# Performance work log

Measured on AMD Instinct MI355X. Metric: run time of the kernel, lower is better.

Reference implementation:

```python
import jax, jax.numpy as jnp
import numpy as np

NEG_SLOPE = 0.2


def _gat_layer(x, src, dst, n, W, a_src, a_dst, b, concat):
    """PyG-style GATConv (inference, self-loops already in src/dst).
    x: [N, Fin]; W: [Fin, H*C]; a_src/a_dst: [H, C]; b: [H*C] or [C]."""
    H, C = a_src.shape
    h = (x @ W).reshape(-1, H, C)                      # [N, H, C]
    al_s = jnp.einsum('nhc,hc->nh', h, a_src)          # [N, H]
    al_d = jnp.einsum('nhc,hc->nh', h, a_dst)          # [N, H]
    e = al_s[src] + al_d[dst]                          # [E, H]
    e = jnp.where(e >= 0, e, NEG_SLOPE * e)            # LeakyReLU(0.2)
    m = jax.ops.segment_max(e, dst, num_segments=n)    # [N, H] softmax over dst
    e = jnp.exp(e - m[dst])
    s = jax.ops.segment_sum(e, dst, num_segments=n)    # [N, H]
    alpha = e / (s[dst] + 1e-16)                       # [E, H]
    msg = h[src] * alpha[:, :, None]                   # [E, H, C]
    out = jax.ops.segment_sum(msg, dst, num_segments=n)  # [N, H, C]
    if concat:
        out = out.reshape(-1, H * C)
    else:
        out = out.mean(axis=1)
    return out + b


def _forward(x, edge_index, W1, as1, ad1, b1, W2, as2, ad2, b2, W3, as3, ad3, b3):
    n = x.shape[0]
    loops = jnp.arange(n, dtype=edge_index.dtype)
    src = jnp.concatenate([edge_index[0], loops])      # add self-loops (PyG default)
    dst = jnp.concatenate([edge_index[1], loops])
    x = _gat_layer(x, src, dst, n, W1, as1, ad1, b1, concat=True)
    x = jax.nn.elu(x)
    x = _gat_layer(x, src, dst, n, W2, as2, ad2, b2, concat=True)
    x = jax.nn.elu(x)
    x = _gat_layer(x, src, dst, n, W3, as3, ad3, b3, concat=False)
    return x


def setup_inputs() -> dict:
    key = jax.random.key(0)
    ks = jax.random.split(key, 16)
    N, E, FIN, HID, H, OUT = 50000, 320000, 256, 64, 4, 64
    sc = 0.1  # keep attention logits in a sane range
    return {
        'x': jax.random.normal(ks[0], (N, FIN), jnp.float32),
        'edge_index': jax.random.randint(ks[1], (2, E), 0, N, jnp.int32),
        'W1': jax.random.normal(ks[2], (FIN, H * HID), jnp.float32) * sc,
        'as1': jax.random.normal(ks[3], (H, HID), jnp.float32) * sc,
        'ad1': jax.random.normal(ks[4], (H, HID), jnp.float32) * sc,
        'b1': jax.random.normal(ks[5], (H * HID,), jnp.float32) * sc,
        'W2': jax.random.normal(ks[6], (H * HID, H * HID), jnp.float32) * sc,
        'as2': jax.random.normal(ks[7], (H, HID), jnp.float32) * sc,
        'ad2': jax.random.normal(ks[8], (H, HID), jnp.float32) * sc,
        'b2': jax.random.normal(ks[9], (H * HID,), jnp.float32) * sc,
        'W3': jax.random.normal(ks[10], (H * HID, OUT), jnp.float32) * sc,
        'as3': jax.random.normal(ks[11], (1, OUT), jnp.float32) * sc,
        'ad3': jax.random.normal(ks[12], (1, OUT), jnp.float32) * sc,
        'b3': jax.random.normal(ks[13], (OUT,), jnp.float32) * sc,
    }


def reference(x, edge_index, W1, as1, ad1, b1, W2, as2, ad2, b2, W3, as3, ad3, b3):
    return _forward(x, edge_index, W1, as1, ad1, b1, W2, as2, ad2, b2, W3, as3, ad3, b3)
```

## Files before the change

### kernel.cpp

```cpp
#include <hip/hip_runtime.h>


typedef __attribute__((ext_vector_type(8))) __bf16 bf16x8;
typedef __attribute__((ext_vector_type(4))) float f32x4;
typedef _Float16 f16x8 __attribute__((ext_vector_type(8)));
typedef _Float16 f16x4 __attribute__((ext_vector_type(4)));

#define NEG_SLOPE 0.2f
#define WELL 40

__device__ __forceinline__ unsigned short f2b_rne(float f) {
    unsigned int u = __float_as_uint(f);
    u += 0x7FFFu + ((u >> 16) & 1u);
    return (unsigned short)(u >> 16);
}
__device__ __forceinline__ unsigned short f2h(float f) {
    _Float16 h = (_Float16)f;
    unsigned short s;
    __builtin_memcpy(&s, &h, 2);
    return s;
}
__device__ __forceinline__ bf16x8 cvt8(const float* f) {
    unsigned short r[8];
#pragma unroll
    for (int j = 0; j < 8; j++) r[j] = f2b_rne(f[j]);
    bf16x8 v;
    __builtin_memcpy(&v, r, 16);
    return v;
}
__device__ __forceinline__ float lrelu(float e) {
    return e >= 0.f ? e : NEG_SLOPE * e;
}

__global__ __launch_bounds__(256) void k_init(const float* __restrict__ W1,
                                              const float* __restrict__ W2,
                                              const float* __restrict__ W3,
                                              unsigned short* __restrict__ W1t,
                                              unsigned short* __restrict__ W2t,
                                              unsigned short* __restrict__ W3t,
                                              int* __restrict__ cnt, int n) {
    int t = blockIdx.x * blockDim.x + threadIdx.x;
    if (t < n) cnt[t] = 0;
    const float* W;
    unsigned short* Wt;
    int Nout, idx = t;
    if (idx < 65536)        { W = W1; Wt = W1t; Nout = 256; }
    else if (idx < 131072)  { W = W2; Wt = W2t; Nout = 256; idx -= 65536; }
    else if (idx < 147456)  { W = W3; Wt = W3t; Nout = 64;  idx -= 131072; }
    else return;
    int k = idx / Nout;
    int c = idx - k * Nout;
    Wt[(size_t)c * 256 + k] = f2b_rne(W[idx]);
}

__global__ __launch_bounds__(256) void k_fillell(const int* __restrict__ src,
                                                 const int* __restrict__ dst,
                                                 int* __restrict__ cnt,
                                                 int* __restrict__ ell, int E) {
    int t = blockIdx.x * blockDim.x + threadIdx.x;
    if (t < E) {
        int d = dst[t];
        int pos = atomicAdd(&cnt[d], 1);
        if (pos < WELL) ell[(size_t)d * WELL + pos] = src[t];
    }
}

template <int NT, bool AF32>
__global__ __launch_bounds__(512) void k_gemm(const void* __restrict__ Av,
                                              const __bf16* __restrict__ Bt,
                                              unsigned short* __restrict__ h16,
                                              float* __restrict__ als,
                                              float* __restrict__ ald,
                                              const float* __restrict__ a_s,
                                              const float* __restrict__ a_d,
                                              int M, int H) {
    constexpr int NN = NT * 16;
    __shared__ __align__(16) __bf16 Bs[NN][256];

    const int tid = threadIdx.x;
    const int lane = tid & 63;
    const int w = tid >> 6;
    const int i = lane & 15;
    const int quad = lane >> 4;
    const int m0 = blockIdx.x * 256;

    {
        int nl = lane >> 5;
        int p = lane & 31;
#pragma unroll
        for (int t = 0; t < NN / 16; t++) {
            int n = t * 16 + w * 2 + nl;
            int g = p ^ (n & 7);
            const __bf16* gp = Bt + (size_t)n * 256 + g * 8;
            __builtin_amdgcn_global_load_lds(
                (const __attribute__((address_space(1))) void*)gp,
                (__attribute__((address_space(3))) void*)&Bs[t * 16 + w * 2][0],
                16, 0, 0);
        }
    }

    int ra = m0 + w * 32 + i;
    int rb = ra + 16;
    if (ra >= M) ra = M - 1;
    if (rb >= M) rb = M - 1;

    bf16x8 afrag[2][8];
    if (AF32) {
        const float* pa = (const float*)Av + (size_t)ra * 256;
        const float* pb = (const float*)Av + (size_t)rb * 256;
#pragma unroll
        for (int half = 0; half < 2; half++) {
            float tmp[2][4][8];
#pragma unroll
            for (int k4 = 0; k4 < 4; k4++) {
                int koff = (half * 4 + k4) * 32 + quad * 8;
                *(float4*)&tmp[0][k4][0] = *(const float4*)(pa + koff);
                *(float4*)&tmp[0][k4][4] = *(const float4*)(pa + koff + 4);
                *(float4*)&tmp[1][k4][0] = *(const float4*)(pb + koff);
                *(float4*)&tmp[1][k4][4] = *(const float4*)(pb + koff + 4);
            }
#pragma unroll
            for (int k4 = 0; k4 < 4; k4++) {
                afrag[0][half * 4 + k4] = cvt8(tmp[0][k4]);
                afrag[1][half * 4 + k4] = cvt8(tmp[1][k4]);
            }
        }
    } else {
        const __bf16* pa = (const __bf16*)Av + (size_t)ra * 256;
        const __bf16* pb = (const __bf16*)Av + (size_t)rb * 256;
#pragma unroll
        for (int kc = 0; kc < 8; kc++) {
            int koff = kc * 32 + quad * 8;
            afrag[0][kc] = *(const bf16x8*)(pa + koff);
            afrag[1][kc] = *(const bf16x8*)(pb + koff);
        }
    }

    f32x4 acc[2][NT] = {};

    __syncthreads();

#pragma unroll
    for (int kc = 0; kc < 8; kc++) {
        const int c = kc * 4 + quad;
#pragma unroll
        for (int nt = 0; nt < NT; nt++) {
            const int n = nt * 16 + i;
            const int p = c ^ (n & 7);
            bf16x8 bfv = *(const bf16x8*)&Bs[n][p * 8];
            acc[0][nt] = __builtin_amdgcn_mfma_f32_16x16x32_bf16(
                afrag[0][kc], bfv, acc[0][nt], 0, 0, 0);
            acc[1][nt] = __builtin_amdgcn_mfma_f32_16x16x32_bf16(
                afrag[1][kc], bfv, acc[1][nt], 0, 0, 0);
        }
    }

    float asv[NT], adv[NT];
#pragma unroll
    for (int nt = 0; nt < NT; nt++) {
        asv[nt] = a_s[(nt / 4) * 64 + (nt & 3) * 16 + i];
        adv[nt] = a_d[(nt / 4) * 64 + (nt & 3) * 16 + i];
    }

#pragma unroll
    for (int mt = 0; mt < 2; mt++) {
#pragma unroll
        for (int r = 0; r < 4; r++) {
            int row = m0 + w * 32 + mt * 16 + quad * 4 + r;
            bool ok = row < M;
#pragma unroll
            for (int nt = 0; nt < NT; nt++) {
                if (ok) h16[(size_t)row * NN + nt * 16 + i] = f2h(acc[mt][nt][r]);
            }
#pragma unroll
            for (int g = 0; g < (NT + 3) / 4; g++) {
                float ps = 0.f, pd = 0.f;
#pragma unroll
                for (int j = 0; j < 4 && g * 4 + j < NT; j++) {
                    float v = acc[mt][g * 4 + j][r];
                    ps += v * asv[g * 4 + j];
                    pd += v * adv[g * 4 + j];
                }
#pragma unroll
                for (int off = 1; off <= 8; off <<= 1) {
                    ps += __shfl_xor(ps, off, 64);
                    pd += __shfl_xor(pd, off, 64);
                }
                if (ok && i == 0) {
                    als[(size_t)row * H + g] = ps;
                    ald[(size_t)row * H + g] = pd;
                }
            }
        }
    }
}

__global__ __launch_bounds__(256) void k_agg4(const unsigned short* __restrict__ h16,
                                              const float* __restrict__ als,
                                              const float* __restrict__ ald,
                                              const int* __restrict__ cnt,
                                              const int* __restrict__ ell,
                                              const float* __restrict__ bias,
                                              unsigned short* __restrict__ xout,
                                              int n) {
    int gw = (blockIdx.x * blockDim.x + threadIdx.x) >> 6;
    int lane = threadIdx.x & 63;
    int wid = gw * 4 + (lane >> 4);
    if (wid >= n) return;
    int l = lane & 15;
    int head = l >> 2;
    int ch = l * 16;
    int base = lane & 48;

    int deg = min(cnt[wid], WELL);
    const int* row = ell + (size_t)wid * WELL;
    int myid = (l < deg) ? row[l] : 0;

    float aldv = ald[wid * 4 + head];
    float p = __expf(fminf(lrelu(als[wid * 4 + head] + aldv), 60.f));
    float ssum = p;
    float a[16];
    {
        f16x8 h0 = *(const f16x8*)&h16[(size_t)wid * 256 + ch];
        f16x8 h1 = *(const f16x8*)&h16[(size_t)wid * 256 + ch + 8];
#pragma unroll
        for (int j = 0; j < 8; j++) { a[j] = p * (float)h0[j]; a[8 + j] = p * (float)h1[j]; }
    }

    int jmax = min(deg, 16);
    int dm1 = deg - 1;
    for (int j = 0; j < jmax; j += 4) {
        int s0 = __shfl(myid, base + min(j, dm1));
        int s1 = __shfl(myid, base + min(j + 1, dm1));
        int s2 = __shfl(myid, base + min(j + 2, dm1));
        int s3 = __shfl(myid, base + min(j + 3, dm1));
        float e0 = als[s0 * 4 + head];
        float e1 = als[s1 * 4 + head];
        float e2 = als[s2 * 4 + head];
        float e3 = als[s3 * 4 + head];
        f16x8 v0a = *(const f16x8*)&h16[(size_t)s0 * 256 + ch];
        f16x8 v0b = *(const f16x8*)&h16[(size_t)s0 * 256 + ch + 8];
        f16x8 v1a = *(const f16x8*)&h16[(size_t)s1 * 256 + ch];
        f16x8 v1b = *(const f16x8*)&h16[(size_t)s1 * 256 + ch + 8];
        f16x8 v2a = *(const f16x8*)&h16[(size_t)s2 * 256 + ch];
        f16x8 v2b = *(const f16x8*)&h16[(size_t)s2 * 256 + ch + 8];
        f16x8 v3a = *(const f16x8*)&h16[(size_t)s3 * 256 + ch];
        f16x8 v3b = *(const f16x8*)&h16[(size_t)s3 * 256 + ch + 8];
        float p0 = __expf(fminf(lrelu(e0 + aldv), 60.f));
        float p1 = (j + 1 < deg) ? __expf(fminf(lrelu(e1 + aldv), 60.f)) : 0.f;
        float p2 = (j + 2 < deg) ? __expf(fminf(lrelu(e2 + aldv), 60.f)) : 0.f;
        float p3 = (j + 3 < deg) ? __expf(fminf(lrelu(e3 + aldv), 60.f)) : 0.f;
        ssum += (p0 + p1) + (p2 + p3);
#pragma unroll
        for (int k = 0; k < 8; k++) {
            a[k]     += (p0 * (float)v0a[k] + p1 * (float)v1a[k]) +
                        (p2 * (float)v2a[k] + p3 * (float)v3a[k]);
            a[8 + k] += (p0 * (float)v0b[k] + p1 * (float)v1b[k]) +
                        (p2 * (float)v2b[k] + p3 * (float)v3b[k]);
        }
    }
    for (int j = 16; j < deg; ++j) {
        int s0 = row[j];
        float p0 = __expf(fminf(lrelu(als[s0 * 4 + head] + aldv), 60.f));
        f16x8 v0a = *(const f16x8*)&h16[(size_t)s0 * 256 + ch];
        f16x8 v0b = *(const f16x8*)&h16[(size_t)s0 * 256 + ch + 8];
        ssum += p0;
#pragma unroll
        for (int k = 0; k < 8; k++) {
            a[k] += p0 * (float)v0a[k];
            a[8 + k] += p0 * (float)v0b[k];
        }
    }

    float inv = 1.f / (ssum + 1e-16f);
    float bb[16];
#pragma unroll
    for (int q = 0; q < 4; q++)
        *(float4*)&bb[q * 4] = *(const float4*)&bias[ch + q * 4];
    unsigned short o[16];
#pragma unroll
    for (int k = 0; k < 16; k++) {
        float r = a[k] * inv + bb[k];
        r = r > 0.f ? r : expm1f(r);
        o[k] = f2b_rne(r);
    }
    *(int4*)&xout[(size_t)wid * 256 + ch] = *(const int4*)&o[0];
    *(int4*)&xout[(size_t)wid * 256 + ch + 8] = *(const int4*)&o[8];
}

__global__ __launch_bounds__(256) void k_agg1(const unsigned short* __restrict__ h16,
                                              const float* __restrict__ als,
                                              const float* __restrict__ ald,
                                              const int* __restrict__ cnt,
                                              const int* __restrict__ ell,
                                              const float* __restrict__ bias,
                                              float* __restrict__ out, int n) {
    int gw = (blockIdx.x * blockDim.x + threadIdx.x) >> 6;
    int lane = threadIdx.x & 63;
    int wid = gw * 4 + (lane >> 4);
    if (wid >= n) return;
    int l = lane & 15;
    int ch = l * 4;
    int base = lane & 48;

    int deg = min(cnt[wid], WELL);
    const int* row = ell + (size_t)wid * WELL;
    int myid = (l < deg) ? row[l] : 0;

    float aldv = ald[wid];
    float p = __expf(fminf(lrelu(als[wid] + aldv), 60.f));
    float ssum = p;
    float a[4];
    {
        f16x4 hv = *(const f16x4*)&h16[(size_t)wid * 64 + ch];
#pragma unroll
        for (int k = 0; k < 4; k++) a[k] = p * (float)hv[k];
    }

    int jmax = min(deg, 16);
    int dm1 = deg - 1;
    for (int j = 0; j < jmax; j += 4) {
        int s0 = __shfl(myid, base + min(j, dm1));
        int s1 = __shfl(myid, base + min(j + 1, dm1));
        int s2 = __shfl(myid, base + min(j + 2, dm1));
        int s3 = __shfl(myid, base + min(j + 3, dm1));
        float e0 = als[s0], e1 = als[s1], e2 = als[s2], e3 = als[s3];
        f16x4 v0 = *(const f16x4*)&h16[(size_t)s0 * 64 + ch];
        f16x4 v1 = *(const f16x4*)&h16[(size_t)s1 * 64 + ch];
        f16x4 v2 = *(const f16x4*)&h16[(size_t)s2 * 64 + ch];
        f16x4 v3 = *(const f16x4*)&h16[(size_t)s3 * 64 + ch];
        float p0 = __expf(fminf(lrelu(e0 + aldv), 60.f));
        float p1 = (j + 1 < deg) ? __expf(fminf(lrelu(e1 + aldv), 60.f)) : 0.f;
        float p2 = (j + 2 < deg) ? __expf(fminf(lrelu(e2 + aldv), 60.f)) : 0.f;
        float p3 = (j + 3 < deg) ? __expf(fminf(lrelu(e3 + aldv), 60.f)) : 0.f;
        ssum += (p0 + p1) + (p2 + p3);
#pragma unroll
        for (int k = 0; k < 4; k++)
            a[k] += (p0 * (float)v0[k] + p1 * (float)v1[k]) +
                    (p2 * (float)v2[k] + p3 * (float)v3[k]);
    }
    for (int j = 16; j < deg; ++j) {
        int s0 = row[j];
        float p0 = __expf(fminf(lrelu(als[s0] + aldv), 60.f));
        f16x4 v0 = *(const f16x4*)&h16[(size_t)s0 * 64 + ch];
        ssum += p0;
#pragma unroll
        for (int k = 0; k < 4; k++) a[k] += p0 * (float)v0[k];
    }
    float inv = 1.f / (ssum + 1e-16f);
    float4 bv = *(const float4*)&bias[ch];
    float4 r;
    r.x = a[0] * inv + bv.x;
    r.y = a[1] * inv + bv.y;
    r.z = a[2] * inv + bv.z;
    r.w = a[3] * inv + bv.w;
    *(float4*)&out[(size_t)wid * 64 + ch] = r;
}

extern "C" void kernel_launch(void* const* d_in, const int* in_sizes, int n_in,
                              void* d_out, int out_size, void* d_ws, size_t ws_size,
                              hipStream_t stream) {
    const float* x   = (const float*)d_in[0];
    const int*   ei  = (const int*)d_in[1];
    const float* W1  = (const float*)d_in[2];
    const float* as1 = (const float*)d_in[3];
    const float* ad1 = (const float*)d_in[4];
    const float* b1  = (const float*)d_in[5];
    const float* W2  = (const float*)d_in[6];
    const float* as2 = (const float*)d_in[7];
    const float* ad2 = (const float*)d_in[8];
    const float* b2  = (const float*)d_in[9];
    const float* W3  = (const float*)d_in[10];
    const float* as3 = (const float*)d_in[11];
    const float* ad3 = (const float*)d_in[12];
    const float* b3  = (const float*)d_in[13];

    const int N = in_sizes[0] / 256;
    const int E = in_sizes[1] / 2;

    size_t off = 0;
    auto alloc = [&](size_t bytes) -> void* {
        void* p = (char*)d_ws + off;
        off += (bytes + 255) & ~(size_t)255;
        return p;
    };
    unsigned short* xb  = (unsigned short*)alloc((size_t)N * 256 * 2);
    unsigned short* W1t = (unsigned short*)alloc((size_t)256 * 256 * 2);
    unsigned short* W2t = (unsigned short*)alloc((size_t)256 * 256 * 2);
    unsigned short* W3t = (unsigned short*)alloc((size_t)64 * 256 * 2);
    unsigned short* h16 = (unsigned short*)alloc((size_t)N * 256 * 2);
    float* als = (float*)alloc((size_t)N * 4 * 4);
    float* ald = (float*)alloc((size_t)N * 4 * 4);
    int* cnt   = (int*)alloc((size_t)N * 4);
    int* ell   = (int*)alloc((size_t)N * WELL * 4);

    const int T = 256;
    const int agg_blocks = (N + 15) / 16;
    const int mtiles = (N + 255) / 256;

    k_init<<<dim3(576), T, 0, stream>>>(W1, W2, W3, W1t, W2t, W3t, cnt, N);

    k_fillell<<<dim3((E + T - 1) / T), T, 0, stream>>>(ei, ei + E, cnt, ell, E);

    k_gemm<16, true><<<dim3(mtiles), 512, 0, stream>>>(x, (const __bf16*)W1t,
                                                       h16, als, ald, as1, ad1, N, 4);
    k_agg4<<<dim3(agg_blocks), T, 0, stream>>>(h16, als, ald, cnt, ell, b1, xb, N);

    k_gemm<16, false><<<dim3(mtiles), 512, 0, stream>>>(xb, (const __bf16*)W2t,
                                                        h16, als, ald, as2, ad2, N, 4);
    k_agg4<<<dim3(agg_blocks), T, 0, stream>>>(h16, als, ald, cnt, ell, b2, xb, N);

    k_gemm<4, false><<<dim3(mtiles), 512, 0, stream>>>(xb, (const __bf16*)W3t,
                                                       h16, als, ald, as3, ad3, N, 1);
    k_agg1<<<dim3(agg_blocks), T, 0, stream>>>(h16, als, ald, cnt, ell, b3,
                                               (float*)d_out, N);
}
```

Baseline: 266.4 us.

## Sort destination nodes by degree bucket to balance aggregation wavefronts

Adds a degree histogram, scan, and permutation pass so that the aggregation kernels process nodes grouped by in-degree, and each 16-lane group within a wavefront handles nodes of similar degree. The aim is to cut divergence, where a wavefront waits on its highest-degree node. In exchange there are three extra small kernel launches plus atomics, an indirection through perm, and less locality in the h16/als/xout accesses because node order is no longer sequential.

```diff
diff --git a/kernel.cpp b/kernel.cpp
--- a/kernel.cpp
+++ b/kernel.cpp
@@ -8,6 +8,7 @@
 
 #define NEG_SLOPE 0.2f
 #define WELL 40
+#define NBUCK 17
 
 __device__ __forceinline__ unsigned short f2b_rne(float f) {
     unsigned int u = __float_as_uint(f);
@@ -38,9 +39,11 @@
                                               unsigned short* __restrict__ W1t,
                                               unsigned short* __restrict__ W2t,
                                               unsigned short* __restrict__ W3t,
-                                              int* __restrict__ cnt, int n) {
+                                              int* __restrict__ cnt,
+                                              int* __restrict__ bcnt, int n) {
     int t = blockIdx.x * blockDim.x + threadIdx.x;
     if (t < n) cnt[t] = 0;
+    if (t < 32) bcnt[t] = 0;
     const float* W;
     unsigned short* Wt;
     int Nout, idx = t;
@@ -62,6 +65,36 @@
         int d = dst[t];
         int pos = atomicAdd(&cnt[d], 1);
         if (pos < WELL) ell[(size_t)d * WELL + pos] = src[t];
+    }
+}
+
+__global__ __launch_bounds__(256) void k_hist(const int* __restrict__ cnt,
+                                              int* __restrict__ bcnt, int n) {
+    __shared__ int sh[NBUCK];
+    if (threadIdx.x < NBUCK) sh[threadIdx.x] = 0;
+    __syncthreads();
+    int i = blockIdx.x * blockDim.x + threadIdx.x;
+    if (i < n) atomicAdd(&sh[min(cnt[i], 16)], 1);
+    __syncthreads();
+    if (threadIdx.x < NBUCK && sh[threadIdx.x]) atomicAdd(&bcnt[threadIdx.x], sh[threadIdx.x]);
+}
+
+__global__ __launch_bounds__(32) void k_scanb(const int* __restrict__ bcnt,
+                                              int* __restrict__ boff) {
+    if (threadIdx.x == 0) {
+        int run = 0;
+#pragma unroll
+        for (int k = 0; k < NBUCK; k++) { boff[k] = run; run += bcnt[k]; }
+    }
+}
+
+__global__ __launch_bounds__(256) void k_perm(const int* __restrict__ cnt,
+                                              int* __restrict__ boff,
+                                              int* __restrict__ perm, int n) {
+    int i = blockIdx.x * blockDim.x + threadIdx.x;
+    if (i < n) {
+        int pos = atomicAdd(&boff[min(cnt[i], 16)], 1);
+        perm[pos] = i;
     }
 }
 
@@ -200,13 +233,15 @@
                                               const float* __restrict__ ald,
                                               const int* __restrict__ cnt,
                                               const int* __restrict__ ell,
+                                              const int* __restrict__ perm,
                                               const float* __restrict__ bias,
                                               unsigned short* __restrict__ xout,
                                               int n) {
     int gw = (blockIdx.x * blockDim.x + threadIdx.x) >> 6;
     int lane = threadIdx.x & 63;
-    int wid = gw * 4 + (lane >> 4);
-    if (wid >= n) return;
+    int idx = gw * 4 + (lane >> 4);
+    if (idx >= n) return;
+    int wid = perm[idx];
     int l = lane & 15;
     int head = l >> 2;
     int ch = l * 16;
@@ -293,12 +328,14 @@
                                               const float* __restrict__ ald,
                                               const int* __restrict__ cnt,
                                               const int* __restrict__ ell,
+                                              const int* __restrict__ perm,
                                               const float* __restrict__ bias,
                                               float* __restrict__ out, int n) {
     int gw = (blockIdx.x * blockDim.x + threadIdx.x) >> 6;
     int lane = threadIdx.x & 63;
-    int wid = gw * 4 + (lane >> 4);
-    if (wid >= n) return;
+    int idx = gw * 4 + (lane >> 4);
+    if (idx >= n) return;
+    int wid = perm[idx];
     int l = lane & 15;
     int ch = l * 4;
     int base = lane & 48;
@@ -393,25 +430,33 @@
     float* ald = (float*)alloc((size_t)N * 4 * 4);
     int* cnt   = (int*)alloc((size_t)N * 4);
     int* ell   = (int*)alloc((size_t)N * WELL * 4);
+    int* bcnt  = (int*)alloc(32 * 4);
+    int* boff  = (int*)alloc(32 * 4);
+    int* perm  = (int*)alloc((size_t)N * 4);
 
     const int T = 256;
+    const int nblocks = (N + T - 1) / T;
     const int agg_blocks = (N + 15) / 16;
     const int mtiles = (N + 255) / 256;
 
-    k_init<<<dim3(576), T, 0, stream>>>(W1, W2, W3, W1t, W2t, W3t, cnt, N);
+    k_init<<<dim3(576), T, 0, stream>>>(W1, W2, W3, W1t, W2t, W3t, cnt, bcnt, N);
 
     k_fillell<<<dim3((E + T - 1) / T), T, 0, stream>>>(ei, ei + E, cnt, ell, E);
+
+    k_hist<<<dim3(nblocks), T, 0, stream>>>(cnt, bcnt, N);
+    k_scanb<<<dim3(1), 32, 0, stream>>>(bcnt, boff);
+    k_perm<<<dim3(nblocks), T, 0, stream>>>(cnt, boff, perm, N);
 
     k_gemm<16, true><<<dim3(mtiles), 512, 0, stream>>>(x, (const __bf16*)W1t,
                                                        h16, als, ald, as1, ad1, N, 4);
-    k_agg4<<<dim3(agg_blocks), T, 0, stream>>>(h16, als, ald, cnt, ell, b1, xb, N);
+    k_agg4<<<dim3(agg_blocks), T, 0, stream>>>(h16, als, ald, cnt, ell, perm, b1, xb, N);
 
     k_gemm<16, false><<<dim3(mtiles), 512, 0, stream>>>(xb, (const __bf16*)W2t,
                                                         h16, als, ald, as2, ad2, N, 4);
-    k_agg4<<<dim3(agg_blocks), T, 0, stream>>>(h16, als, ald, cnt, ell, b2, xb, N);
+    k_agg4<<<dim3(agg_blocks), T, 0, stream>>>(h16, als, ald, cnt, ell, perm, b2, xb, N);
 
     k_gemm<4, false><<<dim3(mtiles), 512, 0, stream>>>(xb, (const __bf16*)W3t,
                                                        h16, als, ald, as3, ad3, N, 1);
-    k_agg1<<<dim3(agg_blocks), T, 0, stream>>>(h16, als, ald, cnt, ell, b3,
+    k_agg1<<<dim3(agg_blocks), T, 0, stream>>>(h16, als, ald, cnt, ell, perm, b3,
                                                (float*)d_out, N);
 }
```

After: 455.3 us. 70.9% more time.
